# Performance work log

Hardware: AMD Instinct MI355X
Metric: run time of the kernel (lower is better)

## Reference

```python
import jax, jax.numpy as jnp
import numpy as np

DECAY = 0.999
EPS = 1e-05
COMMIT = 0.25


def _layer_norm(x, g, b, eps=1e-5):
    mu = x.mean(-1, keepdims=True)
    var = ((x - mu) ** 2).mean(-1, keepdims=True)
    return (x - mu) * jax.lax.rsqrt(var + eps) * g + b


def setup_inputs() -> dict:
    key = jax.random.key(0)
    ks = jax.random.split(key, 8)
    B, T, D, M, H = 8, 4096, 512, 1024, 512
    init_bound = 1.0 / 512
    embedding = jax.random.uniform(ks[0], (M, D), jnp.float32, -init_bound, init_bound)
    return {
        "dense_x": jax.random.normal(ks[1], (B, T, D), jnp.float32),
        "dense_padding_mask": jax.random.randint(ks[2], (B, T), 0, 2).astype(bool),
        "labels": jax.random.randint(ks[3], (B, T), 0, M),
        "embedding": embedding,
        "ema_count": jnp.zeros((M,), jnp.float32),
        "ema_weight": embedding,
        "ln1_g": jnp.ones((D,), jnp.float32),
        "ln1_b": jnp.zeros((D,), jnp.float32),
        "W1": jax.random.normal(ks[4], (D, H), jnp.float32) * (1.0 / np.sqrt(D)),
        "ln2_g": jnp.ones((H,), jnp.float32),
        "ln2_b": jnp.zeros((H,), jnp.float32),
        "W2": jax.random.normal(ks[5], (H, M), jnp.float32) * (1.0 / np.sqrt(H)),
    }


def reference(dense_x, dense_padding_mask, labels, embedding, ema_count, ema_weight,
              ln1_g, ln1_b, W1, ln2_g, ln2_b, W2):
    B, T, D = dense_x.shape
    M = embedding.shape[0]
    N = B * T

    # ---- VQ codebook (EMA) ----
    x_flat = jax.lax.stop_gradient(dense_x).reshape(N, D)
    distances = (jnp.sum(embedding ** 2, axis=1)[None, :]
                 + jnp.sum(x_flat ** 2, axis=1, keepdims=True)
                 - 2.0 * (x_flat @ embedding.T))
    indices = jnp.argmin(distances, axis=-1)  # [N]
    quantized = embedding[indices].reshape(B, T, D)

    # EMA codebook update (training path); encodings.sum(0) and encodings.T @ x
    # expressed as scatter-adds instead of materializing [N, M] one-hot.
    counts = jnp.zeros((M,), dense_x.dtype).at[indices].add(1.0)
    new_count = DECAY * ema_count + (1.0 - DECAY) * counts
    n = jnp.sum(new_count)
    new_count = (new_count + EPS) / (n + M * EPS) * n
    dw = jnp.zeros((M, D), dense_x.dtype).at[indices].add(x_flat)
    new_weight = DECAY * ema_weight + (1.0 - DECAY) * dw
    new_embedding = new_weight / new_count[:, None]

    e_latent_loss = (dense_x - jax.lax.stop_gradient(quantized)) ** 2  # [B,T,D]
    vq_loss = COMMIT * e_latent_loss
    quantized_st = dense_x + jax.lax.stop_gradient(quantized - dense_x)

    avg_probs = counts / N
    perplexity = jnp.exp(-jnp.sum(avg_probs * jnp.log(avg_probs + 1e-10)))

    # ---- decoder: LN -> ReLU -> Linear -> LN -> ReLU -> Linear ----
    h = jax.nn.relu(_layer_norm(dense_x, ln1_g, ln1_b)) @ W1      # [B,T,H]
    logits = jax.nn.relu(_layer_norm(h, ln2_g, ln2_b)) @ W2       # [B,T,M]

    # ---- cross-entropy with ignore_index=-1 (padding) ----
    lab = jnp.where(dense_padding_mask, -1, labels)
    valid = lab >= 0
    safe = jnp.where(valid, lab, 0)
    logp = jax.nn.log_softmax(logits, axis=-1)
    ce = -jnp.take_along_axis(logp, safe[..., None], axis=-1)[..., 0]
    recon_loss = jnp.where(valid, ce, 0.0)

    loss = recon_loss + vq_loss.sum(-1)  # [B,T]
    return quantized_st, loss, perplexity, new_embedding, new_count, new_weight
```

## Files before the change

kernel.cpp:

```cpp
#include <hip/hip_runtime.h>


#define N_TOK 32768
#define WAITV(n) __builtin_amdgcn_s_waitcnt(0x0F70 | (n))
#define BAR() __builtin_amdgcn_s_barrier()

typedef __attribute__((ext_vector_type(8))) short short8;
typedef _Float16 half8 __attribute__((ext_vector_type(8)));
typedef __attribute__((ext_vector_type(4))) float f32x4;

__device__ __forceinline__ f32x4 mfma16(short8 a, short8 b, f32x4 c) {
    return __builtin_amdgcn_mfma_f32_16x16x32_bf16(a, b, c, 0, 0, 0);
}
__device__ __forceinline__ f32x4 mfma16h(half8 a, half8 b, f32x4 c) {
    return __builtin_amdgcn_mfma_f32_16x16x32_f16(a, b, c, 0, 0, 0);
}

__device__ __forceinline__ void gl_lds16(const unsigned short* g, char* l) {
    __builtin_amdgcn_global_load_lds(
        (const __attribute__((address_space(1))) void*)g,
        (__attribute__((address_space(3))) void*)l, 16, 0, 0);
}

__device__ __forceinline__ unsigned short f2bf(float x) {
    unsigned u = __float_as_uint(x);
    u += 0x7fffu + ((u >> 16) & 1u);
    return (unsigned short)(u >> 16);
}
__device__ __forceinline__ float bf2f(unsigned short h) {
    return __uint_as_float(((unsigned)h) << 16);
}
__device__ __forceinline__ unsigned short f2h(float x) {
    union { _Float16 h; unsigned short u; } c;
    c.h = (_Float16)x;
    return c.u;
}
__device__ __forceinline__ float h2f(unsigned short u) {
    union { _Float16 h; unsigned short u; } c;
    c.u = u;
    return (float)c.h;
}

__device__ __forceinline__ float waveSum(float v) {
#pragma unroll
    for (int off = 32; off > 0; off >>= 1) v += __shfl_down(v, off, 64);
    return v;
}
__device__ __forceinline__ float xorSum(float v) {
#pragma unroll
    for (int off = 1; off < 64; off <<= 1) v += __shfl_xor(v, off);
    return v;
}

__global__ __launch_bounds__(256) void prep_x_kernel(
        const float* __restrict__ X, const float* __restrict__ g,
        const float* __restrict__ b, unsigned short* __restrict__ Xf,
        unsigned short* __restrict__ A1, unsigned long long* __restrict__ minpack) {
    int tid = threadIdx.x;
    if (tid < 4) minpack[(blockIdx.x << 2) + tid] = ~0ULL;
    int lane = tid & 63;
    int n = (blockIdx.x << 2) + (tid >> 6);
    const float* row = X + ((size_t)n << 9);
    float v[8]; float s = 0.f, ss = 0.f;
#pragma unroll
    for (int i = 0; i < 8; ++i) { v[i] = row[lane + (i << 6)]; s += v[i]; ss += v[i] * v[i]; }
    s = xorSum(s); ss = xorSum(ss);
    float mu = s * (1.f / 512.f);
    float rs = rsqrtf(ss * (1.f / 512.f) - mu * mu + 1e-5f);
#pragma unroll
    for (int i = 0; i < 8; ++i) {
        int c = lane + (i << 6);
        size_t o = ((size_t)n << 9) + c;
        float x = v[i];
        Xf[o] = f2h(x);
        float a = fmaxf((x - mu) * rs * g[c] + b[c], 0.f);
        A1[o] = f2bf(a);
    }
}

__global__ __launch_bounds__(256) void prep_e_kernel(
        const float* __restrict__ E, unsigned short* __restrict__ Ehf,
        unsigned short* __restrict__ Elf, float* __restrict__ e_sq,
        int* __restrict__ izero) {
    if (blockIdx.x < 8) izero[(blockIdx.x << 8) + threadIdx.x] = 0;
    int lane = threadIdx.x & 63;
    int m = (blockIdx.x << 2) + (threadIdx.x >> 6);
    const float* row = E + ((size_t)m << 9);
    float ss = 0.f;
#pragma unroll
    for (int i = 0; i < 8; ++i) {
        int c = lane + (i << 6);
        float x = row[c];
        ss += x * x;
        float xs = x * 512.f;
        unsigned short h = f2h(xs);
        size_t o = ((size_t)m << 9) + c;
        Ehf[o] = h;
        Elf[o] = f2h(xs - h2f(h));
    }
    ss = xorSum(ss);
    if (lane == 0) e_sq[m] = ss * 512.f;
}

__global__ __launch_bounds__(256) void prep_wt_kernel(
        const float* __restrict__ W1, const float* __restrict__ W2,
        unsigned short* __restrict__ W1T, unsigned short* __restrict__ W2T) {
    __shared__ float t[32][33];
    int bx = blockIdx.x;
    const float* W = (bx < 16) ? W1 : W2;
    unsigned short* WT = (bx < 16) ? W1T : W2T;
    int Nw = (bx < 16) ? 512 : 1024;
    int n0 = ((bx < 16) ? bx : (bx - 16)) << 5, k0 = blockIdx.y << 5;
    int tx = threadIdx.x & 31, ty = threadIdx.x >> 5;
#pragma unroll
    for (int l = 0; l < 4; ++l)
        t[ty + (l << 3)][tx] = W[(size_t)(k0 + ty + (l << 3)) * Nw + n0 + tx];
    __syncthreads();
#pragma unroll
    for (int l = 0; l < 4; ++l)
        WT[(((size_t)(n0 + ty + (l << 3))) << 9) + k0 + tx] = f2bf(t[tx][ty + (l << 3)]);
}

__device__ __forceinline__ unsigned long long packDist(float d, int m) {
    unsigned u = __float_as_uint(d);
    u = (u & 0x80000000u) ? ~u : (u | 0x80000000u);
    return ((unsigned long long)u << 32) | (unsigned)m;
}

__device__ __forceinline__ void dist_body(
        int q, int x, char* LB,
        const unsigned short* __restrict__ Xf,
        const unsigned short* __restrict__ Ehf, const unsigned short* __restrict__ Elf,
        const float* __restrict__ e_sq, unsigned long long* __restrict__ minpack) {
    int tid = threadIdx.x, lane = tid & 63, w = tid >> 6;
    int quad = lane >> 4, lanelo = lane & 15;
    int wm = w >> 1, wn = w & 1;
    int row0 = (((q >> 3) << 3) | x) << 7;
    int m0 = (q & 7) << 7;

    int srow = ((w & 1) << 6) + lane;
    int skoff = (w >> 1) << 4;
    const unsigned short* pX = Xf  + (((size_t)(row0 + srow)) << 9) + skoff;
    const unsigned short* pH = Ehf + (((size_t)(m0  + srow)) << 9) + skoff;
    const unsigned short* pL = Elf + (((size_t)(m0  + srow)) << 9) + skoff;
    char* ldsB = LB + ((w >> 1) << 12) + ((w & 1) << 10) + (lane << 4);
    const char* ra  = LB + (quad << 11) + (((wm << 6) + lanelo) << 4);
    const char* rbh = LB + 8192 + (quad << 11) + (((wn << 6) + lanelo) << 4);

    f32x4 acc[4][4];
#pragma unroll
    for (int i = 0; i < 4; ++i)
#pragma unroll
        for (int j = 0; j < 4; ++j) acc[i][j] = 0.f;

    gl_lds16(pX, ldsB);            gl_lds16(pX + 8, ldsB + 2048);
    gl_lds16(pH, ldsB + 8192);     gl_lds16(pH + 8, ldsB + 10240);
    gl_lds16(pL, ldsB + 16384);    gl_lds16(pL + 8, ldsB + 18432);

#pragma unroll
    for (int it = 0; it < 16; ++it) {
        const int cb = it & 1;
        if (it < 15) {
            const unsigned short* sX = pX + ((it + 1) << 5);
            const unsigned short* sH = pH + ((it + 1) << 5);
            const unsigned short* sL = pL + ((it + 1) << 5);
            char* d = ldsB + (cb ^ 1) * 24576;
            gl_lds16(sX, d);           gl_lds16(sX + 8, d + 2048);
            gl_lds16(sH, d + 8192);    gl_lds16(sH + 8, d + 10240);
            gl_lds16(sL, d + 16384);   gl_lds16(sL + 8, d + 18432);
            WAITV(6);
        } else {
            WAITV(0);
        }
        BAR();
        const char* A  = ra  + cb * 24576;
        const char* Bh = rbh + cb * 24576;
        half8 av[4], bh[4], bl[4];
#pragma unroll
        for (int i = 0; i < 4; ++i) av[i] = *(const half8*)(A + (i << 8));
#pragma unroll
        for (int j = 0; j < 4; ++j) {
            bh[j] = *(const half8*)(Bh + (j << 8));
            bl[j] = *(const half8*)(Bh + 8192 + (j << 8));
        }
#pragma unroll
        for (int i = 0; i < 4; ++i)
#pragma unroll
            for (int j = 0; j < 4; ++j) acc[i][j] = mfma16h(av[i], bh[j], acc[i][j]);
#pragma unroll
        for (int i = 0; i < 4; ++i)
#pragma unroll
            for (int j = 0; j < 4; ++j) acc[i][j] = mfma16h(av[i], bl[j], acc[i][j]);
        BAR();
    }

    float esq[4];
#pragma unroll
    for (int j = 0; j < 4; ++j) esq[j] = e_sq[m0 + (wn << 6) + (j << 4) + lanelo];
#pragma unroll
    for (int i = 0; i < 4; ++i)
#pragma unroll
        for (int r = 0; r < 4; ++r) {
            unsigned long long best = ~0ULL;
#pragma unroll
            for (int j = 0; j < 4; ++j) {
                int code = m0 + (wn << 6) + (j << 4) + lanelo;
                float d = esq[j] - 2.f * acc[i][j][r];
                unsigned long long p = packDist(d, code);
                if (p < best) best = p;
            }
#pragma unroll
            for (int off = 1; off < 16; off <<= 1) {
                unsigned long long q2 = __shfl_xor(best, off);
                if (q2 < best) best = q2;
            }
            if (lanelo == 0) {
                int t = row0 + (wm << 6) + (i << 4) + (quad << 2) + r;
                atomicMin(&minpack[t], best);
            }
        }
}

__device__ __forceinline__ void gemm1_body(
        int g, int x, char* LB,
        const unsigned short* __restrict__ A1, const unsigned short* __restrict__ W1T,
        unsigned short* __restrict__ Hb) {
    int tid = threadIdx.x, lane = tid & 63, w = tid >> 6;
    int quad = lane >> 4, lanelo = lane & 15;
    int wm = w >> 1, wn = w & 1;
    int row0 = (((g >> 2) << 3) | x) << 7;
    int n0 = (g & 3) << 7;

    int srow = ((w & 1) << 6) + lane;
    int skoff = (w >> 1) << 5;
    const unsigned short* pA = A1  + (((size_t)(row0 + srow)) << 9) + skoff;
    const unsigned short* pB = W1T + (((size_t)(n0   + srow)) << 9) + skoff;
    char* ldsB = LB + ((w >> 1) << 13) + ((w & 1) << 10) + (lane << 4);
    const char* ra = LB + (quad << 11) + (((wm << 6) + lanelo) << 4);
    const char* rb = LB + 16384 + (quad << 11) + (((wn << 6) + lanelo) << 4);

    f32x4 acc[4][4];
#pragma unroll
    for (int i = 0; i < 4; ++i)
#pragma unroll
        for (int j = 0; j < 4; ++j) acc[i][j] = 0.f;

    gl_lds16(pA, ldsB);           gl_lds16(pA + 8, ldsB + 2048);
    gl_lds16(pA + 16, ldsB + 4096); gl_lds16(pA + 24, ldsB + 6144);
    gl_lds16(pB, ldsB + 16384);   gl_lds16(pB + 8, ldsB + 18432);
    gl_lds16(pB + 16, ldsB + 20480); gl_lds16(pB + 24, ldsB + 22528);

#pragma unroll
    for (int it = 0; it < 8; ++it) {
        const int cb = it & 1;
        if (it < 7) {
            const unsigned short* sA = pA + ((it + 1) << 6);
            const unsigned short* sB = pB + ((it + 1) << 6);
            char* d = ldsB + (cb ^ 1) * 32768;
            gl_lds16(sA, d);           gl_lds16(sA + 8, d + 2048);
            gl_lds16(sA + 16, d + 4096); gl_lds16(sA + 24, d + 6144);
            gl_lds16(sB, d + 16384);   gl_lds16(sB + 8, d + 18432);
            gl_lds16(sB + 16, d + 20480); gl_lds16(sB + 24, d + 22528);
            WAITV(8);
        } else {
            WAITV(0);
        }
        BAR();
        const char* A = ra + cb * 32768;
        const char* B = rb + cb * 32768;
#pragma unroll
        for (int kk = 0; kk < 2; ++kk) {
            short8 af[4], bf4[4];
#pragma unroll
            for (int i = 0; i < 4; ++i) af[i] = *(const short8*)(A + (kk << 13) + (i << 8));
#pragma unroll
            for (int j = 0; j < 4; ++j) bf4[j] = *(const short8*)(B + (kk << 13) + (j << 8));
#pragma unroll
            for (int i = 0; i < 4; ++i)
#pragma unroll
                for (int j = 0; j < 4; ++j) acc[i][j] = mfma16(af[i], bf4[j], acc[i][j]);
        }
        BAR();
    }
#pragma unroll
    for (int i = 0; i < 4; ++i)
#pragma unroll
        for (int j = 0; j < 4; ++j)
#pragma unroll
            for (int r = 0; r < 4; ++r) {
                int row = row0 + (wm << 6) + (i << 4) + (quad << 2) + r;
                int col = n0 + (wn << 6) + (j << 4) + lanelo;
                Hb[((size_t)row << 9) + col] = f2bf(acc[i][j][r]);
            }
}

__global__ __launch_bounds__(256) void fused1_kernel(
        const unsigned short* __restrict__ Xf,
        const unsigned short* __restrict__ Ehf, const unsigned short* __restrict__ Elf,
        const float* __restrict__ e_sq, unsigned long long* __restrict__ minpack,
        const unsigned short* __restrict__ A1, const unsigned short* __restrict__ W1T,
        unsigned short* __restrict__ Hb) {
    __shared__ __align__(16) char LB[65536];
    int b = blockIdx.x, x = b & 7, m = b >> 3;
    int t = m % 3, g = m / 3;
    if (t < 2) dist_body((g << 1) + t, x, LB, Xf, Ehf, Elf, e_sq, minpack);
    else       gemm1_body(g, x, LB, A1, W1T, Hb);
}

__global__ __launch_bounds__(256) void fused2_kernel(
        const float* __restrict__ X, const float* __restrict__ E,
        const unsigned long long* __restrict__ minpack,
        float* __restrict__ out_q, int* __restrict__ icounts,
        float* __restrict__ vqsum,
        const unsigned short* __restrict__ Hb, const float* __restrict__ g2,
        const float* __restrict__ b2, unsigned short* __restrict__ A2) {
    int nb = blockIdx.x >> 1;
    int lane = threadIdx.x & 63;
    int n = (nb << 2) + (threadIdx.x >> 6);
    if ((blockIdx.x & 1) == 0) {
        int idx = (int)(minpack[n] & 0xFFFFFFFFULL);
        if (lane == 0) atomicAdd(&icounts[idx], 1);
        const float* xr = X + ((size_t)n << 9);
        const float* er = E + ((size_t)idx << 9);
        float s = 0.f;
#pragma unroll
        for (int i = 0; i < 8; ++i) {
            int c = lane + (i << 6);
            float xv = xr[c], q = er[c];
            out_q[((size_t)n << 9) + c] = q;
            float dlt = xv - q;
            s += dlt * dlt;
        }
        s = waveSum(s);
        if (lane == 0) vqsum[n] = 0.25f * s;
    } else {
        const unsigned short* row = Hb + ((size_t)n << 9);
        float v[8]; float s = 0.f, ss = 0.f;
#pragma unroll
        for (int i = 0; i < 8; ++i) { v[i] = bf2f(row[lane + (i << 6)]); s += v[i]; ss += v[i] * v[i]; }
        s = xorSum(s); ss = xorSum(ss);
        float mu = s * (1.f / 512.f);
        float rs = rsqrtf(ss * (1.f / 512.f) - mu * mu + 1e-5f);
#pragma unroll
        for (int i = 0; i < 8; ++i) {
            int c = lane + (i << 6);
            float a = fmaxf((v[i] - mu) * rs * g2[c] + b2[c], 0.f);
            A2[((size_t)n << 9) + c] = f2bf(a);
        }
    }
}

__global__ __launch_bounds__(1024) void codebook_kernel(
        const float* __restrict__ ema_count, const int* __restrict__ icounts,
        float* __restrict__ out_perp, float* __restrict__ out_newcount,
        int* __restrict__ offsets) {
    __shared__ int sc[1024];
    __shared__ float red[16];
    int tid = threadIdx.x;
    int lane = tid & 63, wid = tid >> 6;
    int ic = icounts[tid];
    sc[tid] = ic;
    for (int off = 1; off < 1024; off <<= 1) {
        __syncthreads();
        int v = (tid >= off) ? sc[tid - off] : 0;
        __syncthreads();
        sc[tid] += v;
    }
    offsets[tid] = sc[tid] - ic;
    __syncthreads();

    float cnt = (float)ic;
    float raw = 0.999f * ema_count[tid] + 0.001f * cnt;
    float v = waveSum(raw);
    if (lane == 0) red[wid] = v;
    __syncthreads();
    float nsum = 0.f;
#pragma unroll
    for (int i = 0; i < 16; ++i) nsum += red[i];
    __syncthreads();
    float p = cnt * (1.f / 32768.f);
    float e = p * logf(p + 1e-10f);
    e = waveSum(e);
    if (lane == 0) red[wid] = e;
    __syncthreads();
    float ent = 0.f;
#pragma unroll
    for (int i = 0; i < 16; ++i) ent += red[i];
    float nc = (raw + 1e-5f) / (nsum + 1024.f * 1e-5f) * nsum;
    out_newcount[tid] = nc;
    if (tid == 0) out_perp[0] = expf(-ent);
}

__global__ __launch_bounds__(256) void scatter_kernel(
        const unsigned long long* __restrict__ minpack,
        const int* __restrict__ offsets, int* __restrict__ cursor,
        int* __restrict__ bucket) {
    int n = (blockIdx.x << 8) + threadIdx.x;
    int idx = (int)(minpack[n] & 0xFFFFFFFFULL);
    int pos = atomicAdd(&cursor[idx], 1);
    bucket[offsets[idx] + pos] = n;
}

__device__ __forceinline__ void dw_body(
        int m, char* LB, const float* __restrict__ X,
        const int* __restrict__ bucket, const int* __restrict__ icounts,
        const int* __restrict__ offsets, float* __restrict__ dw) {
    float* comb = (float*)LB;
    int tid = threadIdx.x, lane = tid & 63, w = tid >> 6;
    int cnt = icounts[m], base = offsets[m];
    float acc[8] = {};
    for (int i = w; i < cnt; i += 4) {
        int t = bucket[base + i];
        const float* xr = X + ((size_t)t << 9);
#pragma unroll
        for (int j = 0; j < 8; ++j) acc[j] += xr[lane + (j << 6)];
    }
#pragma unroll
    for (int j = 0; j < 8; ++j) comb[(w << 9) + lane + (j << 6)] = acc[j];
    __syncthreads();
    for (int c = tid; c < 512; c += 256)
        dw[((size_t)m << 9) + c] = comb[c] + comb[512 + c] + comb[1024 + c] + comb[1536 + c];
}

__device__ __forceinline__ void gemm2_body(
        int q, int x, char* LB,
        float (*lmax)[2][64], float (*lsum)[2][64], float* llab, int* slab,
        const unsigned short* __restrict__ A2, const unsigned short* __restrict__ W2T,
        const int* __restrict__ mask, const int* __restrict__ labels,
        float* __restrict__ ws_cmax, float* __restrict__ ws_csum,
        float* __restrict__ ws_lab) {
    int tid = threadIdx.x, lane = tid & 63, w = tid >> 6;
    int quad = lane >> 4, lanelo = lane & 15;
    int wm = w >> 1, wn = w & 1;
    int row0 = (((q >> 3) << 3) | x) << 7;
    int cy = q & 7;
    int c0 = cy << 7;
    if (tid < 128) {
        int mk = mask[row0 + tid];
        slab[tid] = mk ? 0 : labels[row0 + tid];
    }
    __syncthreads();

    int srow = ((w & 1) << 6) + lane;
    int skoff = (w >> 1) << 5;
    const unsigned short* pA = A2  + (((size_t)(row0 + srow)) << 9) + skoff;
    const unsigned short* pB = W2T + (((size_t)(c0   + srow)) << 9) + skoff;
    char* ldsB = LB + ((w >> 1) << 13) + ((w & 1) << 10) + (lane << 4);
    const char* ra = LB + (quad << 11) + (((wm << 6) + lanelo) << 4);
    const char* rb = LB + 16384 + (quad << 11) + (((wn << 6) + lanelo) << 4);

    f32x4 acc[4][4];
#pragma unroll
    for (int i = 0; i < 4; ++i)
#pragma unroll
        for (int j = 0; j < 4; ++j) acc[i][j] = 0.f;

    gl_lds16(pA, ldsB);           gl_lds16(pA + 8, ldsB + 2048);
    gl_lds16(pA + 16, ldsB + 4096); gl_lds16(pA + 24, ldsB + 6144);
    gl_lds16(pB, ldsB + 16384);   gl_lds16(pB + 8, ldsB + 18432);
    gl_lds16(pB + 16, ldsB + 20480); gl_lds16(pB + 24, ldsB + 22528);

#pragma unroll
    for (int it = 0; it < 8; ++it) {
        const int cb = it & 1;
        if (it < 7) {
            const unsigned short* sA = pA + ((it + 1) << 6);
            const unsigned short* sB = pB + ((it + 1) << 6);
            char* d = ldsB + (cb ^ 1) * 32768;
            gl_lds16(sA, d);           gl_lds16(sA + 8, d + 2048);
            gl_lds16(sA + 16, d + 4096); gl_lds16(sA + 24, d + 6144);
            gl_lds16(sB, d + 16384);   gl_lds16(sB + 8, d + 18432);
            gl_lds16(sB + 16, d + 20480); gl_lds16(sB + 24, d + 22528);
            WAITV(8);
        } else {
            WAITV(0);
        }
        BAR();
        const char* A = ra + cb * 32768;
        const char* B = rb + cb * 32768;
#pragma unroll
        for (int kk = 0; kk < 2; ++kk) {
            short8 af[4], bf4[4];
#pragma unroll
            for (int i = 0; i < 4; ++i) af[i] = *(const short8*)(A + (kk << 13) + (i << 8));
#pragma unroll
            for (int j = 0; j < 4; ++j) bf4[j] = *(const short8*)(B + (kk << 13) + (j << 8));
#pragma unroll
            for (int i = 0; i < 4; ++i)
#pragma unroll
                for (int j = 0; j < 4; ++j) acc[i][j] = mfma16(af[i], bf4[j], acc[i][j]);
        }
        BAR();
    }

#pragma unroll
    for (int i = 0; i < 4; ++i)
#pragma unroll
        for (int j = 0; j < 4; ++j)
#pragma unroll
            for (int r = 0; r < 4; ++r) {
                int code = c0 + (wn << 6) + (j << 4) + lanelo;
                int tt = (wm << 6) + (i << 4) + (quad << 2) + r;
                if (code == slab[tt]) llab[tt] = acc[i][j][r];
            }
#pragma unroll
    for (int i = 0; i < 4; ++i)
#pragma unroll
        for (int r = 0; r < 4; ++r) {
            float mx = fmaxf(fmaxf(acc[i][0][r], acc[i][1][r]),
                             fmaxf(acc[i][2][r], acc[i][3][r]));
#pragma unroll
            for (int off = 1; off < 16; off <<= 1) mx = fmaxf(mx, __shfl_xor(mx, off));
            if (lanelo == 0) lmax[wm][wn][(i << 4) + (quad << 2) + r] = mx;
        }
    __syncthreads();
#pragma unroll
    for (int i = 0; i < 4; ++i)
#pragma unroll
        for (int r = 0; r < 4; ++r) {
            int tl = (i << 4) + (quad << 2) + r;
            float cm = fmaxf(lmax[wm][0][tl], lmax[wm][1][tl]);
            float s2 = expf(acc[i][0][r] - cm) + expf(acc[i][1][r] - cm) +
                       expf(acc[i][2][r] - cm) + expf(acc[i][3][r] - cm);
#pragma unroll
            for (int off = 1; off < 16; off <<= 1) s2 += __shfl_xor(s2, off);
            if (lanelo == 0) lsum[wm][wn][tl] = s2;
        }
    __syncthreads();
    if (tid < 128) {
        int wmi = tid >> 6, tl = tid & 63;
        int token = row0 + tid;
        float cm = fmaxf(lmax[wmi][0][tl], lmax[wmi][1][tl]);
        float cs = lsum[wmi][0][tl] + lsum[wmi][1][tl];
        size_t o = ((size_t)cy << 15) + token;
        ws_cmax[o] = cm;
        ws_csum[o] = cs;
        if ((slab[tid] >> 7) == cy) ws_lab[token] = llab[tid];
    }
}

__global__ __launch_bounds__(256) void fused3_kernel(
        const unsigned short* __restrict__ A2, const unsigned short* __restrict__ W2T,
        const int* __restrict__ mask, const int* __restrict__ labels,
        float* __restrict__ ws_cmax, float* __restrict__ ws_csum,
        float* __restrict__ ws_lab,
        const float* __restrict__ X, const int* __restrict__ bucket,
        const int* __restrict__ icounts, const int* __restrict__ offsets,
        float* __restrict__ dw) {
    __shared__ __align__(16) char LB[65536];
    __shared__ float lmax[2][2][64], lsum[2][2][64], llab[128];
    __shared__ int slab[128];
    int b = blockIdx.x, x = b & 7, m = b >> 3;
    int t = m % 3, g = m / 3;
    if (t < 2) gemm2_body((g << 1) + t, x, LB, lmax, lsum, llab, slab,
                          A2, W2T, mask, labels, ws_cmax, ws_csum, ws_lab);
    else       dw_body((g << 3) | x, LB, X, bucket, icounts, offsets, dw);
}

__global__ __launch_bounds__(256) void epilogue_kernel(
        const float* __restrict__ ema_weight, const float* __restrict__ dw,
        const float* __restrict__ newcount, float* __restrict__ out_neww,
        float* __restrict__ out_newemb,
        const float* __restrict__ ws_cmax, const float* __restrict__ ws_csum,
        const float* __restrict__ ws_lab, const int* __restrict__ mask,
        const float* __restrict__ vqsum, float* __restrict__ loss_out) {
    int bx = blockIdx.x;
    if (bx < 2048) {
        int i = (bx << 8) + threadIdx.x;
        float nw = 0.999f * ema_weight[i] + 0.001f * dw[i];
        out_neww[i] = nw;
        out_newemb[i] = nw / newcount[i >> 9];
    } else {
        int n = ((bx - 2048) << 8) + threadIdx.x;
        float m[8], s[8];
#pragma unroll
        for (int c = 0; c < 8; ++c) {
            m[c] = ws_cmax[(c << 15) + n];
            s[c] = ws_csum[(c << 15) + n];
        }
        float gm = m[0];
#pragma unroll
        for (int c = 1; c < 8; ++c) gm = fmaxf(gm, m[c]);
        float se = 0.f;
#pragma unroll
        for (int c = 0; c < 8; ++c) se += s[c] * expf(m[c] - gm);
        float ce = -(ws_lab[n] - gm - logf(se));
        loss_out[n] = (mask[n] ? 0.f : ce) + vqsum[n];
    }
}

extern "C" void kernel_launch(void* const* d_in, const int* in_sizes, int n_in,
                              void* d_out, int out_size, void* d_ws, size_t ws_size,
                              hipStream_t stream) {
    const float* X          = (const float*)d_in[0];
    const int*   mask       = (const int*)d_in[1];
    const int*   labels     = (const int*)d_in[2];
    const float* E          = (const float*)d_in[3];
    const float* ema_count  = (const float*)d_in[4];
    const float* ema_weight = (const float*)d_in[5];
    const float* g1 = (const float*)d_in[6];
    const float* b1 = (const float*)d_in[7];
    const float* W1 = (const float*)d_in[8];
    const float* g2 = (const float*)d_in[9];
    const float* b2 = (const float*)d_in[10];
    const float* W2 = (const float*)d_in[11];

    float* out = (float*)d_out;
    float* out_q        = out;
    float* out_loss     = out + 16777216;
    float* out_perp     = out + 16809984;
    float* out_newemb   = out + 16809985;
    float* out_newcount = out + 17334273;
    float* out_neww     = out + 17335297;

    float* w = (float*)d_ws;
    float* vqsum = w;  w += 32768;
    float* e_sq = w;   w += 1024;
    float* dwbuf = w;  w += 524288;
    unsigned long long* minpack = (unsigned long long*)w; w += 65536;
    float* ws_cmax = w; w += 262144;
    float* ws_csum = w; w += 262144;
    float* ws_lab  = w; w += 32768;
    int* icounts = (int*)w; w += 1024;
    int* cursor  = (int*)w; w += 1024;
    int* offsets = (int*)w; w += 1024;
    int* bucket  = (int*)w; w += 32768;
    unsigned short* Ehf = (unsigned short*)w; w += 262144;
    unsigned short* Elf = (unsigned short*)w; w += 262144;
    unsigned short* W1T = (unsigned short*)w; w += 131072;
    unsigned short* W2T = (unsigned short*)w; w += 262144;
    unsigned short* Xf  = (unsigned short*)w; w += 8388608;
    unsigned short* A1  = (unsigned short*)w; w += 8388608;
    unsigned short* Hb  = (unsigned short*)w; w += 8388608;
    unsigned short* A2  = Xf;

    prep_e_kernel<<<256, 256, 0, stream>>>(E, Ehf, Elf, e_sq, icounts);
    prep_wt_kernel<<<dim3(48, 16), 256, 0, stream>>>(W1, W2, W1T, W2T);
    prep_x_kernel<<<8192, 256, 0, stream>>>(X, g1, b1, Xf, A1, minpack);
    fused1_kernel<<<3072, 256, 0, stream>>>(Xf, Ehf, Elf, e_sq, minpack,
                                            A1, W1T, Hb);
    fused2_kernel<<<16384, 256, 0, stream>>>(X, E, minpack, out_q, icounts,
                                             vqsum, Hb, g2, b2, A2);
    codebook_kernel<<<1, 1024, 0, stream>>>(ema_count, icounts, out_perp,
                                            out_newcount, offsets);
    scatter_kernel<<<128, 256, 0, stream>>>(minpack, offsets, cursor, bucket);
    fused3_kernel<<<3072, 256, 0, stream>>>(A2, W2T, mask, labels,
                                            ws_cmax, ws_csum, ws_lab,
                                            X, bucket, icounts, offsets, dwbuf);
    epilogue_kernel<<<2176, 256, 0, stream>>>(ema_weight, dwbuf, out_newcount,
                                              out_neww, out_newemb,
                                              ws_cmax, ws_csum, ws_lab,
                                              mask, vqsum, out_loss);
}
```

Measured before the change: 480.5 us.

## Switch GEMM and distance loops to triple-buffered LDS prefetch with smaller K-steps

The distance kernel and both bf16 GEMMs move from double-buffered LDS staging to a three-stage ring, prefetching two K-slices ahead. The GEMMs also drop from K=64 to K=32 per iteration, and their loops are merged into a shared gemm_core helper. The aim is to hide global-to-LDS latency better and to shrink GEMM LDS use, which drops from 64KB to 48KB in fused3. The cost is more barriers per GEMM and a larger 72KB LDS buffer in fused1, which may reduce occupancy there.

```diff
diff --git a/kernel.cpp b/kernel.cpp
--- a/kernel.cpp
+++ b/kernel.cpp
@@ -153,21 +153,31 @@
 #pragma unroll
         for (int j = 0; j < 4; ++j) acc[i][j] = 0.f;
 
-    gl_lds16(pX, ldsB);            gl_lds16(pX + 8, ldsB + 2048);
-    gl_lds16(pH, ldsB + 8192);     gl_lds16(pH + 8, ldsB + 10240);
-    gl_lds16(pL, ldsB + 16384);    gl_lds16(pL + 8, ldsB + 18432);
+#pragma unroll
+    for (int p = 0; p < 2; ++p) {
+        char* d = ldsB + p * 24576;
+        const unsigned short* sX = pX + (p << 5);
+        const unsigned short* sH = pH + (p << 5);
+        const unsigned short* sL = pL + (p << 5);
+        gl_lds16(sX, d);            gl_lds16(sX + 8, d + 2048);
+        gl_lds16(sH, d + 8192);     gl_lds16(sH + 8, d + 10240);
+        gl_lds16(sL, d + 16384);    gl_lds16(sL + 8, d + 18432);
+    }
 
 #pragma unroll
     for (int it = 0; it < 16; ++it) {
-        const int cb = it & 1;
-        if (it < 15) {
-            const unsigned short* sX = pX + ((it + 1) << 5);
-            const unsigned short* sH = pH + ((it + 1) << 5);
-            const unsigned short* sL = pL + ((it + 1) << 5);
-            char* d = ldsB + (cb ^ 1) * 24576;
-            gl_lds16(sX, d);           gl_lds16(sX + 8, d + 2048);
-            gl_lds16(sH, d + 8192);    gl_lds16(sH + 8, d + 10240);
-            gl_lds16(sL, d + 16384);   gl_lds16(sL + 8, d + 18432);
+        const int cb = it % 3;
+        if (it < 14) {
+            const int nb = (it + 2) % 3;
+            const unsigned short* sX = pX + ((it + 2) << 5);
+            const unsigned short* sH = pH + ((it + 2) << 5);
+            const unsigned short* sL = pL + ((it + 2) << 5);
+            char* d = ldsB + nb * 24576;
+            gl_lds16(sX, d);            gl_lds16(sX + 8, d + 2048);
+            gl_lds16(sH, d + 8192);     gl_lds16(sH + 8, d + 10240);
+            gl_lds16(sL, d + 16384);    gl_lds16(sL + 8, d + 18432);
+            WAITV(12);
+        } else if (it == 14) {
             WAITV(6);
         } else {
             WAITV(0);
@@ -219,6 +229,56 @@
                 atomicMin(&minpack[t], best);
             }
         }
+}
+
+__device__ __forceinline__ void gemm_core(
+        char* LB, const unsigned short* pA, const unsigned short* pB,
+        int w, int lane, int quad, int lanelo, int wm, int wn,
+        f32x4 (*acc)[4], bool bf) {
+    char* ldsB = LB + ((w >> 1) << 12) + ((w & 1) << 10) + (lane << 4);
+    const char* ra = LB + (quad << 11) + (((wm << 6) + lanelo) << 4);
+    const char* rb = LB + 8192 + (quad << 11) + (((wn << 6) + lanelo) << 4);
+
+#pragma unroll
+    for (int p = 0; p < 2; ++p) {
+        char* d = ldsB + p * 16384;
+        const unsigned short* sA = pA + (p << 5);
+        const unsigned short* sB = pB + (p << 5);
+        gl_lds16(sA, d);            gl_lds16(sA + 8, d + 2048);
+        gl_lds16(sB, d + 8192);     gl_lds16(sB + 8, d + 10240);
+    }
+
+#pragma unroll
+    for (int it = 0; it < 16; ++it) {
+        const int cb = it % 3;
+        if (it < 14) {
+            const int nb = (it + 2) % 3;
+            const unsigned short* sA = pA + ((it + 2) << 5);
+            const unsigned short* sB = pB + ((it + 2) << 5);
+            char* d = ldsB + nb * 16384;
+            gl_lds16(sA, d);            gl_lds16(sA + 8, d + 2048);
+            gl_lds16(sB, d + 8192);     gl_lds16(sB + 8, d + 10240);
+            WAITV(8);
+        } else if (it == 14) {
+            WAITV(4);
+        } else {
+            WAITV(0);
+        }
+        BAR();
+        const char* A = ra + cb * 16384;
+        const char* B = rb + cb * 16384;
+        short8 af[4], bf4[4];
+#pragma unroll
+        for (int i = 0; i < 4; ++i) af[i] = *(const short8*)(A + (i << 8));
+#pragma unroll
+        for (int j = 0; j < 4; ++j) bf4[j] = *(const short8*)(B + (j << 8));
+#pragma unroll
+        for (int i = 0; i < 4; ++i)
+#pragma unroll
+            for (int j = 0; j < 4; ++j) acc[i][j] = mfma16(af[i], bf4[j], acc[i][j]);
+        BAR();
+    }
+    (void)bf;
 }
 
 __device__ __forceinline__ void gemm1_body(
@@ -232,12 +292,9 @@
     int n0 = (g & 3) << 7;
 
     int srow = ((w & 1) << 6) + lane;
-    int skoff = (w >> 1) << 5;
+    int skoff = (w >> 1) << 4;
     const unsigned short* pA = A1  + (((size_t)(row0 + srow)) << 9) + skoff;
     const unsigned short* pB = W1T + (((size_t)(n0   + srow)) << 9) + skoff;
-    char* ldsB = LB + ((w >> 1) << 13) + ((w & 1) << 10) + (lane << 4);
-    const char* ra = LB + (quad << 11) + (((wm << 6) + lanelo) << 4);
-    const char* rb = LB + 16384 + (quad << 11) + (((wn << 6) + lanelo) << 4);
 
     f32x4 acc[4][4];
 #pragma unroll
@@ -245,43 +302,8 @@
 #pragma unroll
         for (int j = 0; j < 4; ++j) acc[i][j] = 0.f;
 
-    gl_lds16(pA, ldsB);           gl_lds16(pA + 8, ldsB + 2048);
-    gl_lds16(pA + 16, ldsB + 4096); gl_lds16(pA + 24, ldsB + 6144);
-    gl_lds16(pB, ldsB + 16384);   gl_lds16(pB + 8, ldsB + 18432);
-    gl_lds16(pB + 16, ldsB + 20480); gl_lds16(pB + 24, ldsB + 22528);
-
-#pragma unroll
-    for (int it = 0; it < 8; ++it) {
-        const int cb = it & 1;
-        if (it < 7) {
-            const unsigned short* sA = pA + ((it + 1) << 6);
-            const unsigned short* sB = pB + ((it + 1) << 6);
-            char* d = ldsB + (cb ^ 1) * 32768;
-            gl_lds16(sA, d);           gl_lds16(sA + 8, d + 2048);
-            gl_lds16(sA + 16, d + 4096); gl_lds16(sA + 24, d + 6144);
-            gl_lds16(sB, d + 16384);   gl_lds16(sB + 8, d + 18432);
-            gl_lds16(sB + 16, d + 20480); gl_lds16(sB + 24, d + 22528);
-            WAITV(8);
-        } else {
-            WAITV(0);
-        }
-        BAR();
-        const char* A = ra + cb * 32768;
-        const char* B = rb + cb * 32768;
-#pragma unroll
-        for (int kk = 0; kk < 2; ++kk) {
-            short8 af[4], bf4[4];
-#pragma unroll
-            for (int i = 0; i < 4; ++i) af[i] = *(const short8*)(A + (kk << 13) + (i << 8));
-#pragma unroll
-            for (int j = 0; j < 4; ++j) bf4[j] = *(const short8*)(B + (kk << 13) + (j << 8));
-#pragma unroll
-            for (int i = 0; i < 4; ++i)
-#pragma unroll
-                for (int j = 0; j < 4; ++j) acc[i][j] = mfma16(af[i], bf4[j], acc[i][j]);
-        }
-        BAR();
-    }
+    gemm_core(LB, pA, pB, w, lane, quad, lanelo, wm, wn, acc, true);
+
 #pragma unroll
     for (int i = 0; i < 4; ++i)
 #pragma unroll
@@ -300,7 +322,7 @@
         const float* __restrict__ e_sq, unsigned long long* __restrict__ minpack,
         const unsigned short* __restrict__ A1, const unsigned short* __restrict__ W1T,
         unsigned short* __restrict__ Hb) {
-    __shared__ __align__(16) char LB[65536];
+    __shared__ __align__(16) char LB[73728];
     int b = blockIdx.x, x = b & 7, m = b >> 3;
     int t = m % 3, g = m / 3;
     if (t < 2) dist_body((g << 1) + t, x, LB, Xf, Ehf, Elf, e_sq, minpack);
@@ -442,12 +464,9 @@
     __syncthreads();
 
     int srow = ((w & 1) << 6) + lane;
-    int skoff = (w >> 1) << 5;
+    int skoff = (w >> 1) << 4;
     const unsigned short* pA = A2  + (((size_t)(row0 + srow)) << 9) + skoff;
     const unsigned short* pB = W2T + (((size_t)(c0   + srow)) << 9) + skoff;
-    char* ldsB = LB + ((w >> 1) << 13) + ((w & 1) << 10) + (lane << 4);
-    const char* ra = LB + (quad << 11) + (((wm << 6) + lanelo) << 4);
-    const char* rb = LB + 16384 + (quad << 11) + (((wn << 6) + lanelo) << 4);
 
     f32x4 acc[4][4];
 #pragma unroll
@@ -455,43 +474,7 @@
 #pragma unroll
         for (int j = 0; j < 4; ++j) acc[i][j] = 0.f;
 
-    gl_lds16(pA, ldsB);           gl_lds16(pA + 8, ldsB + 2048);
-    gl_lds16(pA + 16, ldsB + 4096); gl_lds16(pA + 24, ldsB + 6144);
-    gl_lds16(pB, ldsB + 16384);   gl_lds16(pB + 8, ldsB + 18432);
-    gl_lds16(pB + 16, ldsB + 20480); gl_lds16(pB + 24, ldsB + 22528);
-
-#pragma unroll
-    for (int it = 0; it < 8; ++it) {
-        const int cb = it & 1;
-        if (it < 7) {
-            const unsigned short* sA = pA + ((it + 1) << 6);
-            const unsigned short* sB = pB + ((it + 1) << 6);
-            char* d = ldsB + (cb ^ 1) * 32768;
-            gl_lds16(sA, d);           gl_lds16(sA + 8, d + 2048);
-            gl_lds16(sA + 16, d + 4096); gl_lds16(sA + 24, d + 6144);
-            gl_lds16(sB, d + 16384);   gl_lds16(sB + 8, d + 18432);
-            gl_lds16(sB + 16, d + 20480); gl_lds16(sB + 24, d + 22528);
-            WAITV(8);
-        } else {
-            WAITV(0);
-        }
-        BAR();
-        const char* A = ra + cb * 32768;
-        const char* B = rb + cb * 32768;
-#pragma unroll
-        for (int kk = 0; kk < 2; ++kk) {
-            short8 af[4], bf4[4];
-#pragma unroll
-            for (int i = 0; i < 4; ++i) af[i] = *(const short8*)(A + (kk << 13) + (i << 8));
-#pragma unroll
-            for (int j = 0; j < 4; ++j) bf4[j] = *(const short8*)(B + (kk << 13) + (j << 8));
-#pragma unroll
-            for (int i = 0; i < 4; ++i)
-#pragma unroll
-                for (int j = 0; j < 4; ++j) acc[i][j] = mfma16(af[i], bf4[j], acc[i][j]);
-        }
-        BAR();
-    }
+    gemm_core(LB, pA, pB, w, lane, quad, lanelo, wm, wn, acc, true);
 
 #pragma unroll
     for (int i = 0; i < 4; ++i)
@@ -547,7 +530,7 @@
         const float* __restrict__ X, const int* __restrict__ bucket,
         const int* __restrict__ icounts, const int* __restrict__ offsets,
         float* __restrict__ dw) {
-    __shared__ __align__(16) char LB[65536];
+    __shared__ __align__(16) char LB[49152];
     __shared__ float lmax[2][2][64], lsum[2][2][64], llab[128];
     __shared__ int slab[128];
     int b = blockIdx.x, x = b & 7, m = b >> 3;
```

Result: no change. 481.4 us (+0.2%).
